# Kernel optimization log

Hardware: AMD Instinct MI355X
Metric: run time of the kernel (lower is better)

## Reference

```python
import jax, jax.numpy as jnp
import numpy as np

HEADS = 16
LN_EPS = 1e-12
MINUS_INF = -10000.0  # matches DeepSpeed's minus_inf constant


def setup_inputs() -> dict:
    key = jax.random.key(0)
    ks = jax.random.split(key, 6)
    B, S, H = 2, 2048, 2048
    x = jax.random.normal(ks[0], (B, S, H), dtype=jnp.float32)
    mask = jnp.zeros((B, 1, 1, S), dtype=jnp.float32)  # additive float mask (no padding)
    qkvw = jax.random.normal(ks[1], (H, 3 * H), dtype=jnp.float32) * 0.02
    qkvb = jax.random.normal(ks[2], (3 * H,), dtype=jnp.float32) * 0.02
    ow = jax.random.normal(ks[3], (H, H), dtype=jnp.float32) * 0.02
    norm_w = jnp.ones((H,), dtype=jnp.float32)
    norm_b = jnp.zeros((H,), dtype=jnp.float32)
    return {"x": x, "mask": mask, "qkvw": qkvw, "qkvb": qkvb, "ow": ow,
            "norm_w": norm_w, "norm_b": norm_b}


def _layernorm(x, g, b):
    mu = jnp.mean(x, axis=-1, keepdims=True)
    var = jnp.mean(jnp.square(x - mu), axis=-1, keepdims=True)
    return (x - mu) * jax.lax.rsqrt(var + LN_EPS) * g + b


def reference(x, mask, qkvw, qkvb, ow, norm_w, norm_b):
    B, S, H = x.shape
    dh = H // HEADS
    # QKVGemmOp: fused layernorm + QKV projection
    inp_norm = _layernorm(x, norm_w, norm_b)                      # [B,S,H]
    qkv = jnp.einsum('bsh,he->bse', inp_norm, qkvw) + qkvb        # [B,S,3H]
    q, k, v = jnp.split(qkv, 3, axis=-1)
    q = q.reshape(B, S, HEADS, dh).transpose(0, 2, 1, 3)          # [B,Hd,S,dh]
    k = k.reshape(B, S, HEADS, dh).transpose(0, 2, 1, 3)
    v = v.reshape(B, S, HEADS, dh).transpose(0, 2, 1, 3)
    # SoftmaxContextOp: kernel scales q and k each by 1/norm_factor,
    # norm_factor = d_head**0.25 (use_mup=False) -> net scale 1/sqrt(d_head)
    scale = 1.0 / jnp.sqrt(jnp.asarray(dh, dtype=x.dtype))
    scores = jnp.einsum('bhqd,bhkd->bhqk', q, k) * scale          # [B,Hd,S,S]
    causal = jnp.tril(jnp.ones((S, S), dtype=bool))
    scores = jnp.where(causal[None, None], scores + mask, MINUS_INF)
    probs = jax.nn.softmax(scores, axis=-1)
    ctx = jnp.einsum('bhqk,bhkd->bhqd', probs, v)                 # [B,Hd,S,dh]
    ctx = ctx.transpose(0, 2, 1, 3).reshape(B, S, H)
    # VectorMatMulOp: output projection (no bias here)
    out = jnp.einsum('bsh,ho->bso', ctx, ow)                      # [B,S,H]
    return (out, k, v, ctx, inp_norm)
```

## Files before the change

kernel.cpp:

```cpp
#include <hip/hip_runtime.h>

typedef short bf16x8 __attribute__((ext_vector_type(8)));
typedef float floatx4 __attribute__((ext_vector_type(4)));

#define MFMA16(a, b, c) __builtin_amdgcn_mfma_f32_16x16x32_bf16((a), (b), (c), 0, 0, 0)

__device__ __forceinline__ unsigned short f2bf(float f) {
    union { float f; unsigned int u; } v; v.f = f;
    unsigned int u = v.u;
    return (unsigned short)((u + 0x7FFFu + ((u >> 16) & 1u)) >> 16);
}

__device__ __forceinline__ void gld_lds16(const void* g, void* l) {
    __builtin_amdgcn_global_load_lds(
        (const __attribute__((address_space(1))) unsigned int*)g,
        (__attribute__((address_space(3))) unsigned int*)l, 16, 0, 0);
}

__global__ __launch_bounds__(256) void ln_kernel(
        const float* __restrict__ x, const float* __restrict__ g,
        const float* __restrict__ be, float* __restrict__ yo,
        unsigned short* __restrict__ yb) {
    int row = blockIdx.x, t = threadIdx.x;
    const float* xr = x + (size_t)row * 2048;
    float4 a = ((const float4*)xr)[2 * t];
    float4 b = ((const float4*)xr)[2 * t + 1];
    float s = a.x + a.y + a.z + a.w + b.x + b.y + b.z + b.w;
    float q = a.x * a.x + a.y * a.y + a.z * a.z + a.w * a.w +
              b.x * b.x + b.y * b.y + b.z * b.z + b.w * b.w;
    for (int m = 1; m < 64; m <<= 1) { s += __shfl_xor(s, m); q += __shfl_xor(q, m); }
    __shared__ float red[8];
    if ((t & 63) == 0) { red[t >> 6] = s; red[4 + (t >> 6)] = q; }
    __syncthreads();
    s = red[0] + red[1] + red[2] + red[3];
    q = red[4] + red[5] + red[6] + red[7];
    float mean = s * (1.0f / 2048.0f);
    float var = q * (1.0f / 2048.0f) - mean * mean;
    float rs = rsqrtf(var + 1e-12f);
    float4 g0 = ((const float4*)g)[2 * t], g1 = ((const float4*)g)[2 * t + 1];
    float4 b0 = ((const float4*)be)[2 * t], b1 = ((const float4*)be)[2 * t + 1];
    float4 y0, y1;
    y0.x = (a.x - mean) * rs * g0.x + b0.x;
    y0.y = (a.y - mean) * rs * g0.y + b0.y;
    y0.z = (a.z - mean) * rs * g0.z + b0.z;
    y0.w = (a.w - mean) * rs * g0.w + b0.w;
    y1.x = (b.x - mean) * rs * g1.x + b1.x;
    y1.y = (b.y - mean) * rs * g1.y + b1.y;
    y1.z = (b.z - mean) * rs * g1.z + b1.z;
    y1.w = (b.w - mean) * rs * g1.w + b1.w;
    float* yr = yo + (size_t)row * 2048;
    ((float4*)yr)[2 * t] = y0;
    ((float4*)yr)[2 * t + 1] = y1;
    union { unsigned short u[8]; uint4 v; } pk;
    pk.u[0] = f2bf(y0.x); pk.u[1] = f2bf(y0.y); pk.u[2] = f2bf(y0.z); pk.u[3] = f2bf(y0.w);
    pk.u[4] = f2bf(y1.x); pk.u[5] = f2bf(y1.y); pk.u[6] = f2bf(y1.z); pk.u[7] = f2bf(y1.w);
    *(uint4*)(yb + (size_t)row * 2048 + t * 8) = pk.v;
}

__global__ __launch_bounds__(256) void transpose_cvt(
        const float* __restrict__ src, unsigned short* __restrict__ dst,
        int K, int N) {
    __shared__ unsigned short tile[64][73];
    int n0 = blockIdx.x * 64, k0 = blockIdx.y * 64;
    size_t bo = (size_t)blockIdx.z * K * N;
    int t = threadIdx.x;
    for (int p = 0; p < 4; p++) {
        int idx = p * 256 + t; int r = idx >> 4; int c = (idx & 15) * 4;
        float4 v = *(const float4*)(src + bo + (size_t)(k0 + r) * N + n0 + c);
        tile[r][c] = f2bf(v.x); tile[r][c + 1] = f2bf(v.y);
        tile[r][c + 2] = f2bf(v.z); tile[r][c + 3] = f2bf(v.w);
    }
    __syncthreads();
    for (int p = 0; p < 4; p++) {
        int idx = p * 256 + t; int n = idx >> 4; int c = (idx & 15) * 4;
        ushort4 o;
        o.x = tile[c][n]; o.y = tile[c + 1][n];
        o.z = tile[c + 2][n]; o.w = tile[c + 3][n];
        *(ushort4*)(dst + bo + (size_t)(n0 + n) * K + k0 + c) = o;
    }
}

#define NT_QKV 32

__device__ __forceinline__ void stage_A(const unsigned short* __restrict__ Ag,
        unsigned short* As, int mh, int m0, int kt, int tid) {
#pragma unroll
    for (int j = 0; j < 2; j++) {
        int G = j * 512 + tid;
        int s = (G >> 3) & 63;
        int gr = G & 7;
        int row = j * 128 + mh * 64 + s;
        const unsigned short* src =
            Ag + (size_t)(m0 + row) * 2048 + kt * 64 + ((gr ^ (s & 7)) << 3);
        unsigned short* dst = As + j * 8192 + mh * 4096 + (tid >> 6) * 512;
        gld_lds16(src, dst);
    }
}

__device__ __forceinline__ void stage_B(const unsigned short* __restrict__ Bg,
        unsigned short* Bs, int nh, int n0, int kt, int tid) {
#pragma unroll
    for (int j = 0; j < 2; j++) {
        int G = j * 512 + tid;
        int wcc = G >> 8;
        int s = (G >> 3) & 31;
        int gr = G & 7;
        int row = wcc * 64 + nh * 32 + s;
        const unsigned short* src =
            Bg + (size_t)(n0 + row) * 2048 + kt * 64 + ((gr ^ (s & 7)) << 3);
        unsigned short* dst = Bs + wcc * 4096 + nh * 2048 + ((tid >> 6) & 3) * 512;
        gld_lds16(src, dst);
    }
}

__device__ __forceinline__ bf16x8 ldfrag(const unsigned short* S, int row, int ks,
                                         int quad, int ln15) {
    int gr = ((ks << 2) | quad) ^ (ln15 & 7);
    return *(const bf16x8*)(S + row * 64 + gr * 8);
}

#define PHASE_SYNC()                                        \
    __builtin_amdgcn_s_barrier();                           \
    asm volatile("s_waitcnt lgkmcnt(0)" ::: "memory");      \
    __builtin_amdgcn_sched_barrier(0);                      \
    __builtin_amdgcn_s_setprio(1)

#define PHASE_END()                                         \
    __builtin_amdgcn_s_setprio(0);                          \
    asm volatile("s_waitcnt vmcnt(4)" ::: "memory");        \
    __builtin_amdgcn_s_barrier()

__device__ __forceinline__ void qkv_tile(
        const unsigned short* __restrict__ Ag, const unsigned short* __restrict__ Bg,
        unsigned short* Asc, unsigned short* Bsc,
        unsigned short* Asn, unsigned short* Bsn,
        int t, int m0, int n0, int tid, int wr, int wc, int ln15, int quad,
        floatx4 (&acc)[8][4]) {
    bf16x8 a[4][2], bb[2][2];
    bool pf = (t + 1 < NT_QKV);
#pragma unroll
    for (int m = 0; m < 4; m++) {
        a[m][0] = ldfrag(Asc, wr * 128 + m * 16 + ln15, 0, quad, ln15);
        a[m][1] = ldfrag(Asc, wr * 128 + m * 16 + ln15, 1, quad, ln15);
    }
#pragma unroll
    for (int n = 0; n < 2; n++) {
        bb[n][0] = ldfrag(Bsc, wc * 64 + n * 16 + ln15, 0, quad, ln15);
        bb[n][1] = ldfrag(Bsc, wc * 64 + n * 16 + ln15, 1, quad, ln15);
    }
    if (pf) stage_B(Bg, Bsn, 0, n0, t + 1, tid);
    PHASE_SYNC();
#pragma unroll
    for (int m = 0; m < 4; m++)
#pragma unroll
        for (int n = 0; n < 2; n++) {
            acc[m][n] = MFMA16(a[m][0], bb[n][0], acc[m][n]);
            acc[m][n] = MFMA16(a[m][1], bb[n][1], acc[m][n]);
        }
    PHASE_END();
#pragma unroll
    for (int n = 0; n < 2; n++) {
        bb[n][0] = ldfrag(Bsc, wc * 64 + (2 + n) * 16 + ln15, 0, quad, ln15);
        bb[n][1] = ldfrag(Bsc, wc * 64 + (2 + n) * 16 + ln15, 1, quad, ln15);
    }
    if (pf) stage_A(Ag, Asn, 0, m0, t + 1, tid);
    PHASE_SYNC();
#pragma unroll
    for (int m = 0; m < 4; m++)
#pragma unroll
        for (int n = 0; n < 2; n++) {
            acc[m][2 + n] = MFMA16(a[m][0], bb[n][0], acc[m][2 + n]);
            acc[m][2 + n] = MFMA16(a[m][1], bb[n][1], acc[m][2 + n]);
        }
    PHASE_END();
#pragma unroll
    for (int m = 0; m < 4; m++) {
        a[m][0] = ldfrag(Asc, wr * 128 + (4 + m) * 16 + ln15, 0, quad, ln15);
        a[m][1] = ldfrag(Asc, wr * 128 + (4 + m) * 16 + ln15, 1, quad, ln15);
    }
    if (pf) stage_B(Bg, Bsn, 1, n0, t + 1, tid);
    PHASE_SYNC();
#pragma unroll
    for (int m = 0; m < 4; m++)
#pragma unroll
        for (int n = 0; n < 2; n++) {
            acc[4 + m][2 + n] = MFMA16(a[m][0], bb[n][0], acc[4 + m][2 + n]);
            acc[4 + m][2 + n] = MFMA16(a[m][1], bb[n][1], acc[4 + m][2 + n]);
        }
    PHASE_END();
#pragma unroll
    for (int n = 0; n < 2; n++) {
        bb[n][0] = ldfrag(Bsc, wc * 64 + n * 16 + ln15, 0, quad, ln15);
        bb[n][1] = ldfrag(Bsc, wc * 64 + n * 16 + ln15, 1, quad, ln15);
    }
    if (pf) stage_A(Ag, Asn, 1, m0, t + 1, tid);
    PHASE_SYNC();
#pragma unroll
    for (int m = 0; m < 4; m++)
#pragma unroll
        for (int n = 0; n < 2; n++) {
            acc[4 + m][n] = MFMA16(a[m][0], bb[n][0], acc[4 + m][n]);
            acc[4 + m][n] = MFMA16(a[m][1], bb[n][1], acc[4 + m][n]);
        }
    PHASE_END();
}

__global__ __launch_bounds__(512, 2) void gemm_qkv(
        const unsigned short* __restrict__ A, const unsigned short* __restrict__ Bt,
        const float* __restrict__ bias, float* __restrict__ ko,
        float* __restrict__ vo, unsigned short* __restrict__ qws,
        unsigned short* __restrict__ kbf) {
    __shared__ __align__(16) unsigned short As[2][16384];
    __shared__ __align__(16) unsigned short Bs[2][16384];
    int bid = blockIdx.x;
    int xcd = bid & 7, idx = bid >> 3;
    int mt = (xcd & 3) * 4 + idx / 12;
    int ntile = (xcd >> 2) * 12 + idx % 12;
    int m0 = mt * 256, n0 = ntile * 256;
    int tid = threadIdx.x;
    int wave = tid >> 6, lane = tid & 63, ln15 = lane & 15, quad = lane >> 4;
    int wr = wave >> 2, wc = wave & 3;
    floatx4 acc[8][4] = {};
    stage_B(Bt, Bs[0], 0, n0, 0, tid);
    stage_A(A, As[0], 0, m0, 0, tid);
    stage_B(Bt, Bs[0], 1, n0, 0, tid);
    stage_A(A, As[0], 1, m0, 0, tid);
    asm volatile("s_waitcnt vmcnt(4)" ::: "memory");
    __builtin_amdgcn_s_barrier();
#pragma unroll 1
    for (int t = 0; t < NT_QKV; t += 2) {
        qkv_tile(A, Bt, As[0], Bs[0], As[1], Bs[1], t,     m0, n0, tid, wr, wc, ln15, quad, acc);
        qkv_tile(A, Bt, As[1], Bs[1], As[0], Bs[0], t + 1, m0, n0, tid, wr, wc, ln15, quad, acc);
    }
#pragma unroll
    for (int mi = 0; mi < 8; mi++) {
        int row = m0 + wr * 128 + mi * 16 + quad * 4;
#pragma unroll
        for (int ni = 0; ni < 4; ni++) {
            int col = n0 + wc * 64 + ni * 16 + ln15;
            float bv = bias[col];
#pragma unroll
            for (int r = 0; r < 4; r++) {
                float val = acc[mi][ni][r] + bv;
                int rr = row + r;
                int b = rr >> 11, s = rr & 2047;
                if (col < 2048) {
                    qws[(size_t)rr * 2048 + col] = f2bf(val);
                } else if (col < 4096) {
                    int cc = col - 2048; int h = cc >> 7, d = cc & 127;
                    size_t o = ((size_t)(b * 16 + h) * 2048 + s) * 128 + d;
                    ko[o] = val;
                    kbf[o] = f2bf(val);
                } else {
                    int cc = col - 4096; int h = cc >> 7, d = cc & 127;
                    vo[((size_t)(b * 16 + h) * 2048 + s) * 128 + d] = val;
                }
            }
        }
    }
}

__global__ __launch_bounds__(256) void gemm_out(
        const float* __restrict__ Actx, const unsigned short* __restrict__ Bt,
        float* __restrict__ out) {
    __shared__ unsigned short As[128 * 72];
    __shared__ unsigned short Bs[128 * 72];
    int m0 = blockIdx.y * 128, n0 = blockIdx.x * 128;
    int t = threadIdx.x;
    int wave = t >> 6, lane = t & 63, ln15 = lane & 15, quad = lane >> 4;
    int wm = wave >> 1, wn = wave & 1;
    floatx4 acc[4][4] = {};
    for (int k0 = 0; k0 < 2048; k0 += 64) {
        for (int p = 0; p < 4; p++) {
            int idx = p * 256 + t; int r = idx >> 3; int c = (idx & 7) * 8;
            const float* ap = Actx + (size_t)(m0 + r) * 2048 + k0 + c;
            float4 u0 = ((const float4*)ap)[0], u1 = ((const float4*)ap)[1];
            union { unsigned short u[8]; uint4 v; } pk;
            pk.u[0] = f2bf(u0.x); pk.u[1] = f2bf(u0.y); pk.u[2] = f2bf(u0.z); pk.u[3] = f2bf(u0.w);
            pk.u[4] = f2bf(u1.x); pk.u[5] = f2bf(u1.y); pk.u[6] = f2bf(u1.z); pk.u[7] = f2bf(u1.w);
            *(uint4*)&As[r * 72 + c] = pk.v;
            *(uint4*)&Bs[r * 72 + c] = *(const uint4*)(Bt + (size_t)(n0 + r) * 2048 + k0 + c);
        }
        __syncthreads();
        for (int ks = 0; ks < 2; ks++) {
            bf16x8 af[4], bfr[4];
            for (int i = 0; i < 4; i++)
                af[i] = *(const bf16x8*)&As[(wm * 64 + i * 16 + ln15) * 72 + ks * 32 + quad * 8];
            for (int i = 0; i < 4; i++)
                bfr[i] = *(const bf16x8*)&Bs[(wn * 64 + i * 16 + ln15) * 72 + ks * 32 + quad * 8];
            for (int mi = 0; mi < 4; mi++)
                for (int ni = 0; ni < 4; ni++)
                    acc[mi][ni] = MFMA16(af[mi], bfr[ni], acc[mi][ni]);
        }
        __syncthreads();
    }
    for (int mi = 0; mi < 4; mi++) {
        int row = m0 + wm * 64 + mi * 16 + quad * 4;
        for (int ni = 0; ni < 4; ni++) {
            int col = n0 + wn * 64 + ni * 16 + ln15;
            for (int r = 0; r < 4; r++)
                out[(size_t)(row + r) * 2048 + col] = acc[mi][ni][r];
        }
    }
}

__global__ __launch_bounds__(256) void attn_kernel(
        const unsigned short* __restrict__ qws, const unsigned short* __restrict__ kbf,
        const unsigned short* __restrict__ vT, const float* __restrict__ mask,
        float* __restrict__ ctxo) {
    __shared__ unsigned short Ks[64 * 136];
    __shared__ unsigned short Vt[128 * 72];
    __shared__ unsigned short Pl[4 * 16 * 72];
    int jp = blockIdx.x, h = blockIdx.y, b = blockIdx.z;
    int t = threadIdx.x, wave = t >> 6, lane = t & 63, ln15 = lane & 15, quad = lane >> 4;
    const float scale = 0.08838834764831845f;

    const unsigned short* kb = kbf + (size_t)(b * 16 + h) * 2048 * 128;
    const unsigned short* vTb = vT + (size_t)(b * 16 + h) * 128 * 2048;
    const float* mb = mask + (size_t)b * 2048;

    for (int half = 0; half < 2; half++) {
        int qt = half ? (31 - jp) : jp;
        int Q0 = qt * 64;

        bf16x8 qf[4];
        const unsigned short* qbase =
            qws + ((size_t)(b * 2048 + Q0 + wave * 16 + ln15)) * 2048 + h * 128;
        for (int ks = 0; ks < 4; ks++)
            qf[ks] = *(const bf16x8*)(qbase + ks * 32 + quad * 8);

        float m_r[4], l_r[4];
        floatx4 o[8] = {};
        for (int r = 0; r < 4; r++) { m_r[r] = -1e30f; l_r[r] = 0.0f; }

        int nkt = qt + 1;
        for (int kt = 0; kt < nkt; kt++) {
            int c0 = kt * 64;
            for (int p = 0; p < 4; p++) {
                int idx = p * 256 + t; int r = idx >> 4; int c = (idx & 15) * 8;
                *(uint4*)&Ks[r * 136 + c] = *(const uint4*)(kb + (size_t)(c0 + r) * 128 + c);
            }
            for (int p = 0; p < 4; p++) {
                int idx = p * 256 + t; int d = idx >> 3; int sg = (idx & 7) * 8;
                *(uint4*)&Vt[d * 72 + sg] = *(const uint4*)(vTb + (size_t)d * 2048 + c0 + sg);
            }
            __syncthreads();

            floatx4 cs[4] = {};
            for (int ks = 0; ks < 4; ks++)
                for (int ni = 0; ni < 4; ni++) {
                    bf16x8 kfr = *(const bf16x8*)&Ks[(ni * 16 + ln15) * 136 + ks * 32 + quad * 8];
                    cs[ni] = MFMA16(qf[ks], kfr, cs[ni]);
                }

            float sv[4][4];
            float mt[4] = {-1e30f, -1e30f, -1e30f, -1e30f};
            if (kt == qt) {
                for (int ni = 0; ni < 4; ni++) {
                    int cg = c0 + ni * 16 + ln15;
                    float mk = mb[cg];
                    for (int r = 0; r < 4; r++) {
                        int qg = Q0 + wave * 16 + quad * 4 + r;
                        float v = (cg <= qg) ? cs[ni][r] * scale + mk : -10000.0f;
                        sv[ni][r] = v;
                        mt[r] = fmaxf(mt[r], v);
                    }
                }
            } else {
                for (int ni = 0; ni < 4; ni++) {
                    float mk = mb[c0 + ni * 16 + ln15];
                    for (int r = 0; r < 4; r++) {
                        float v = cs[ni][r] * scale + mk;
                        sv[ni][r] = v;
                        mt[r] = fmaxf(mt[r], v);
                    }
                }
            }
            for (int m = 1; m < 16; m <<= 1)
                for (int r = 0; r < 4; r++) mt[r] = fmaxf(mt[r], __shfl_xor(mt[r], m));
            float alpha[4], lt[4];
            for (int r = 0; r < 4; r++) {
                float mn = fmaxf(m_r[r], mt[r]);
                alpha[r] = __expf(m_r[r] - mn);
                m_r[r] = mn;
                lt[r] = 0.0f;
            }
            for (int ni = 0; ni < 4; ni++)
                for (int r = 0; r < 4; r++) {
                    float p = __expf(sv[ni][r] - m_r[r]);
                    sv[ni][r] = p;
                    lt[r] += p;
                }
            for (int m = 1; m < 16; m <<= 1)
                for (int r = 0; r < 4; r++) lt[r] += __shfl_xor(lt[r], m);
            for (int r = 0; r < 4; r++) l_r[r] = l_r[r] * alpha[r] + lt[r];
            for (int nj = 0; nj < 8; nj++)
                for (int r = 0; r < 4; r++) o[nj][r] *= alpha[r];

            unsigned short* pw = &Pl[wave * 16 * 72];
            for (int ni = 0; ni < 4; ni++)
                for (int r = 0; r < 4; r++)
                    pw[(quad * 4 + r) * 72 + ni * 16 + ln15] = f2bf(sv[ni][r]);

            for (int ks2 = 0; ks2 < 2; ks2++) {
                bf16x8 pf = *(const bf16x8*)&Pl[(wave * 16 + ln15) * 72 + ks2 * 32 + quad * 8];
                for (int nj = 0; nj < 8; nj++) {
                    bf16x8 vf = *(const bf16x8*)&Vt[(nj * 16 + ln15) * 72 + ks2 * 32 + quad * 8];
                    o[nj] = MFMA16(pf, vf, o[nj]);
                }
            }
            __syncthreads();
        }

        float rl[4];
        for (int r = 0; r < 4; r++) rl[r] = 1.0f / l_r[r];
        for (int nj = 0; nj < 8; nj++)
            for (int r = 0; r < 4; r++) {
                int s = Q0 + wave * 16 + quad * 4 + r;
                ctxo[((size_t)(b * 2048 + s)) * 2048 + h * 128 + nj * 16 + ln15] = o[nj][r] * rl[r];
            }
    }
}

extern "C" void kernel_launch(void* const* d_in, const int* in_sizes, int n_in,
                              void* d_out, int out_size, void* d_ws, size_t ws_size,
                              hipStream_t stream) {
    const float* x      = (const float*)d_in[0];
    const float* mask   = (const float*)d_in[1];
    const float* qkvw   = (const float*)d_in[2];
    const float* qkvb   = (const float*)d_in[3];
    const float* ow     = (const float*)d_in[4];
    const float* norm_w = (const float*)d_in[5];
    const float* norm_b = (const float*)d_in[6];

    float* out      = (float*)d_out;
    float* k_out    = out + 8388608;
    float* v_out    = out + 16777216;
    float* ctx_out  = out + 25165824;
    float* norm_out = out + 33554432;

    unsigned short* ws    = (unsigned short*)d_ws;
    unsigned short* xn    = ws;
    unsigned short* qkvwT = ws + 8388608;
    unsigned short* owT   = ws + 8388608 + 12582912;
    unsigned short* qws   = owT + 4194304;
    unsigned short* vT    = qws + 8388608;
    unsigned short* kbf   = vT + 8388608;

    ln_kernel<<<4096, 256, 0, stream>>>(x, norm_w, norm_b, norm_out, xn);
    transpose_cvt<<<dim3(96, 32, 1), 256, 0, stream>>>(qkvw, qkvwT, 2048, 6144);
    transpose_cvt<<<dim3(32, 32, 1), 256, 0, stream>>>(ow, owT, 2048, 2048);
    gemm_qkv<<<dim3(384), 512, 0, stream>>>(xn, qkvwT, qkvb, k_out, v_out, qws, kbf);
    transpose_cvt<<<dim3(2, 32, 32), 256, 0, stream>>>(v_out, vT, 2048, 128);
    attn_kernel<<<dim3(16, 16, 2), 256, 0, stream>>>(qws, kbf, vT, mask, ctx_out);
    gemm_out<<<dim3(16, 32), 256, 0, stream>>>(ctx_out, owT, out);
}
```

Measured before the change: 551.3 us.

## Restructure attention kernel with 128-row query tiles, register prefetch, lazy rescale

```diff
diff --git a/kernel.cpp b/kernel.cpp
--- a/kernel.cpp
+++ b/kernel.cpp
@@ -304,120 +304,186 @@
     }
 }
 
-__global__ __launch_bounds__(256) void attn_kernel(
+__device__ __forceinline__ void load_kv(const unsigned short* __restrict__ kb,
+                                        const unsigned short* __restrict__ vTb,
+                                        int c0, int t, uint4 (&kg)[4], uint4 (&vg)[4]) {
+#pragma unroll
+    for (int p = 0; p < 4; p++) {
+        int idx = p * 256 + t;
+        int r = idx >> 4, c = (idx & 15) * 8;
+        kg[p] = *(const uint4*)(kb + (size_t)(c0 + r) * 128 + c);
+        int d = idx >> 3, sg = (idx & 7) * 8;
+        vg[p] = *(const uint4*)(vTb + (size_t)d * 2048 + c0 + sg);
+    }
+}
+
+__global__ __launch_bounds__(256, 2) void attn_kernel(
         const unsigned short* __restrict__ qws, const unsigned short* __restrict__ kbf,
         const unsigned short* __restrict__ vT, const float* __restrict__ mask,
         float* __restrict__ ctxo) {
     __shared__ unsigned short Ks[64 * 136];
     __shared__ unsigned short Vt[128 * 72];
-    __shared__ unsigned short Pl[4 * 16 * 72];
-    int jp = blockIdx.x, h = blockIdx.y, b = blockIdx.z;
+    __shared__ unsigned short Pl[4 * 32 * 72];
+    int j = 15 - (int)blockIdx.x, h = blockIdx.y, b = blockIdx.z;
     int t = threadIdx.x, wave = t >> 6, lane = t & 63, ln15 = lane & 15, quad = lane >> 4;
     const float scale = 0.08838834764831845f;
 
     const unsigned short* kb = kbf + (size_t)(b * 16 + h) * 2048 * 128;
     const unsigned short* vTb = vT + (size_t)(b * 16 + h) * 128 * 2048;
     const float* mb = mask + (size_t)b * 2048;
-
-    for (int half = 0; half < 2; half++) {
-        int qt = half ? (31 - jp) : jp;
-        int Q0 = qt * 64;
-
-        bf16x8 qf[4];
+    int Q0 = j * 128;
+
+    bf16x8 qf[2][4];
+#pragma unroll
+    for (int g = 0; g < 2; g++) {
         const unsigned short* qbase =
-            qws + ((size_t)(b * 2048 + Q0 + wave * 16 + ln15)) * 2048 + h * 128;
+            qws + ((size_t)(b * 2048 + Q0 + wave * 32 + g * 16 + ln15)) * 2048 + h * 128;
+#pragma unroll
         for (int ks = 0; ks < 4; ks++)
-            qf[ks] = *(const bf16x8*)(qbase + ks * 32 + quad * 8);
-
-        float m_r[4], l_r[4];
-        floatx4 o[8] = {};
-        for (int r = 0; r < 4; r++) { m_r[r] = -1e30f; l_r[r] = 0.0f; }
-
-        int nkt = qt + 1;
-        for (int kt = 0; kt < nkt; kt++) {
-            int c0 = kt * 64;
-            for (int p = 0; p < 4; p++) {
-                int idx = p * 256 + t; int r = idx >> 4; int c = (idx & 15) * 8;
-                *(uint4*)&Ks[r * 136 + c] = *(const uint4*)(kb + (size_t)(c0 + r) * 128 + c);
+            qf[g][ks] = *(const bf16x8*)(qbase + ks * 32 + quad * 8);
+    }
+
+    float m_r[2][4], l_r[2][4];
+    floatx4 o[2][8] = {};
+#pragma unroll
+    for (int g = 0; g < 2; g++)
+#pragma unroll
+        for (int r = 0; r < 4; r++) { m_r[g][r] = -1e30f; l_r[g][r] = 0.0f; }
+
+    int nkt = 2 * j + 2;
+    uint4 kg[4], vg[4];
+    load_kv(kb, vTb, 0, t, kg, vg);
+
+#pragma unroll 1
+    for (int kt = 0; kt < nkt; kt++) {
+        int c0 = kt * 64;
+        __syncthreads();
+#pragma unroll
+        for (int p = 0; p < 4; p++) {
+            int idx = p * 256 + t;
+            int r = idx >> 4, c = (idx & 15) * 8;
+            *(uint4*)&Ks[r * 136 + c] = kg[p];
+            int d = idx >> 3, sg = (idx & 7) * 8;
+            *(uint4*)&Vt[d * 72 + sg] = vg[p];
+        }
+        __syncthreads();
+        if (kt + 1 < nkt) load_kv(kb, vTb, c0 + 64, t, kg, vg);
+
+        floatx4 cs[2][4] = {};
+        __builtin_amdgcn_s_setprio(1);
+#pragma unroll
+        for (int ks = 0; ks < 4; ks++) {
+            bf16x8 k0 = *(const bf16x8*)&Ks[(0 * 16 + ln15) * 136 + ks * 32 + quad * 8];
+            bf16x8 k1 = *(const bf16x8*)&Ks[(1 * 16 + ln15) * 136 + ks * 32 + quad * 8];
+            bf16x8 k2 = *(const bf16x8*)&Ks[(2 * 16 + ln15) * 136 + ks * 32 + quad * 8];
+            bf16x8 k3 = *(const bf16x8*)&Ks[(3 * 16 + ln15) * 136 + ks * 32 + quad * 8];
+#pragma unroll
+            for (int g = 0; g < 2; g++) {
+                cs[g][0] = MFMA16(qf[g][ks], k0, cs[g][0]);
+                cs[g][1] = MFMA16(qf[g][ks], k1, cs[g][1]);
+                cs[g][2] = MFMA16(qf[g][ks], k2, cs[g][2]);
+                cs[g][3] = MFMA16(qf[g][ks], k3, cs[g][3]);
             }
-            for (int p = 0; p < 4; p++) {
-                int idx = p * 256 + t; int d = idx >> 3; int sg = (idx & 7) * 8;
-                *(uint4*)&Vt[d * 72 + sg] = *(const uint4*)(vTb + (size_t)d * 2048 + c0 + sg);
-            }
-            __syncthreads();
-
-            floatx4 cs[4] = {};
-            for (int ks = 0; ks < 4; ks++)
-                for (int ni = 0; ni < 4; ni++) {
-                    bf16x8 kfr = *(const bf16x8*)&Ks[(ni * 16 + ln15) * 136 + ks * 32 + quad * 8];
-                    cs[ni] = MFMA16(qf[ks], kfr, cs[ni]);
-                }
-
-            float sv[4][4];
-            float mt[4] = {-1e30f, -1e30f, -1e30f, -1e30f};
-            if (kt == qt) {
-                for (int ni = 0; ni < 4; ni++) {
-                    int cg = c0 + ni * 16 + ln15;
-                    float mk = mb[cg];
-                    for (int r = 0; r < 4; r++) {
-                        int qg = Q0 + wave * 16 + quad * 4 + r;
-                        float v = (cg <= qg) ? cs[ni][r] * scale + mk : -10000.0f;
-                        sv[ni][r] = v;
-                        mt[r] = fmaxf(mt[r], v);
-                    }
-                }
-            } else {
-                for (int ni = 0; ni < 4; ni++) {
-                    float mk = mb[c0 + ni * 16 + ln15];
-                    for (int r = 0; r < 4; r++) {
-                        float v = cs[ni][r] * scale + mk;
-                        sv[ni][r] = v;
-                        mt[r] = fmaxf(mt[r], v);
-                    }
+        }
+        __builtin_amdgcn_s_setprio(0);
+
+        float mt[2][4];
+#pragma unroll
+        for (int g = 0; g < 2; g++) {
+#pragma unroll
+            for (int r = 0; r < 4; r++) mt[g][r] = -1e30f;
+#pragma unroll
+            for (int ni = 0; ni < 4; ni++) {
+                int cg = c0 + ni * 16 + ln15;
+                float mk = mb[cg];
+#pragma unroll
+                for (int r = 0; r < 4; r++) {
+                    int qg = Q0 + wave * 32 + g * 16 + quad * 4 + r;
+                    float v = fmaf(cs[g][ni][r], scale, mk);
+                    v = (cg <= qg) ? v : -10000.0f;
+                    cs[g][ni][r] = v;
+                    mt[g][r] = fmaxf(mt[g][r], v);
                 }
             }
+#pragma unroll
             for (int m = 1; m < 16; m <<= 1)
-                for (int r = 0; r < 4; r++) mt[r] = fmaxf(mt[r], __shfl_xor(mt[r], m));
-            float alpha[4], lt[4];
-            for (int r = 0; r < 4; r++) {
-                float mn = fmaxf(m_r[r], mt[r]);
-                alpha[r] = __expf(m_r[r] - mn);
-                m_r[r] = mn;
-                lt[r] = 0.0f;
-            }
+#pragma unroll
+                for (int r = 0; r < 4; r++)
+                    mt[g][r] = fmaxf(mt[g][r], __shfl_xor(mt[g][r], m));
+        }
+
+        bool grow = false;
+#pragma unroll
+        for (int g = 0; g < 2; g++)
+#pragma unroll
+            for (int r = 0; r < 4; r++)
+                grow = grow || (mt[g][r] > m_r[g][r] + 8.0f);
+        if (__any((int)grow)) {
+#pragma unroll
+            for (int g = 0; g < 2; g++)
+#pragma unroll
+                for (int r = 0; r < 4; r++) {
+                    float mn = fmaxf(m_r[g][r], mt[g][r]);
+                    float alpha = __expf(m_r[g][r] - mn);
+                    m_r[g][r] = mn;
+                    l_r[g][r] *= alpha;
+#pragma unroll
+                    for (int nj = 0; nj < 8; nj++) o[g][nj][r] *= alpha;
+                }
+        }
+
+#pragma unroll
+        for (int g = 0; g < 2; g++) {
+            float lt[4] = {0.0f, 0.0f, 0.0f, 0.0f};
+#pragma unroll
             for (int ni = 0; ni < 4; ni++)
+#pragma unroll
                 for (int r = 0; r < 4; r++) {
-                    float p = __expf(sv[ni][r] - m_r[r]);
-                    sv[ni][r] = p;
+                    float p = __expf(cs[g][ni][r] - m_r[g][r]);
+                    cs[g][ni][r] = p;
                     lt[r] += p;
                 }
+#pragma unroll
             for (int m = 1; m < 16; m <<= 1)
+#pragma unroll
                 for (int r = 0; r < 4; r++) lt[r] += __shfl_xor(lt[r], m);
-            for (int r = 0; r < 4; r++) l_r[r] = l_r[r] * alpha[r] + lt[r];
-            for (int nj = 0; nj < 8; nj++)
-                for (int r = 0; r < 4; r++) o[nj][r] *= alpha[r];
-
-            unsigned short* pw = &Pl[wave * 16 * 72];
+#pragma unroll
+            for (int r = 0; r < 4; r++) l_r[g][r] += lt[r];
+            unsigned short* pw = &Pl[(wave * 32 + g * 16) * 72];
+#pragma unroll
             for (int ni = 0; ni < 4; ni++)
+#pragma unroll
                 for (int r = 0; r < 4; r++)
-                    pw[(quad * 4 + r) * 72 + ni * 16 + ln15] = f2bf(sv[ni][r]);
-
-            for (int ks2 = 0; ks2 < 2; ks2++) {
-                bf16x8 pf = *(const bf16x8*)&Pl[(wave * 16 + ln15) * 72 + ks2 * 32 + quad * 8];
-                for (int nj = 0; nj < 8; nj++) {
-                    bf16x8 vf = *(const bf16x8*)&Vt[(nj * 16 + ln15) * 72 + ks2 * 32 + quad * 8];
-                    o[nj] = MFMA16(pf, vf, o[nj]);
-                }
+                    pw[(quad * 4 + r) * 72 + ni * 16 + ln15] = f2bf(cs[g][ni][r]);
+        }
+
+        __builtin_amdgcn_s_setprio(1);
+#pragma unroll
+        for (int ks2 = 0; ks2 < 2; ks2++) {
+            bf16x8 pf0 = *(const bf16x8*)&Pl[(wave * 32 + 0 * 16 + ln15) * 72 + ks2 * 32 + quad * 8];
+            bf16x8 pf1 = *(const bf16x8*)&Pl[(wave * 32 + 1 * 16 + ln15) * 72 + ks2 * 32 + quad * 8];
+#pragma unroll
+            for (int nj = 0; nj < 8; nj++) {
+                bf16x8 vf = *(const bf16x8*)&Vt[(nj * 16 + ln15) * 72 + ks2 * 32 + quad * 8];
+                o[0][nj] = MFMA16(pf0, vf, o[0][nj]);
+                o[1][nj] = MFMA16(pf1, vf, o[1][nj]);
             }
-            __syncthreads();
-        }
-
+        }
+        __builtin_amdgcn_s_setprio(0);
+    }
+
+#pragma unroll
+    for (int g = 0; g < 2; g++) {
         float rl[4];
-        for (int r = 0; r < 4; r++) rl[r] = 1.0f / l_r[r];
+#pragma unroll
+        for (int r = 0; r < 4; r++) rl[r] = 1.0f / l_r[g][r];
+#pragma unroll
         for (int nj = 0; nj < 8; nj++)
+#pragma unroll
             for (int r = 0; r < 4; r++) {
-                int s = Q0 + wave * 16 + quad * 4 + r;
-                ctxo[((size_t)(b * 2048 + s)) * 2048 + h * 128 + nj * 16 + ln15] = o[nj][r] * rl[r];
+                int s = Q0 + wave * 32 + g * 16 + quad * 4 + r;
+                ctxo[((size_t)(b * 2048 + s)) * 2048 + h * 128 + nj * 16 + ln15] =
+                    o[g][nj][r] * rl[r];
             }
     }
 }
```

Result: slower. 682.0 us (+23.7%).

## Prefetch next K/V tile into registers and skip lazy softmax rescales

Applied to the files above, without the earlier changes.

```diff
diff --git a/kernel.cpp b/kernel.cpp
--- a/kernel.cpp
+++ b/kernel.cpp
@@ -304,7 +304,20 @@
     }
 }
 
-__global__ __launch_bounds__(256) void attn_kernel(
+__device__ __forceinline__ void load_kv(const unsigned short* __restrict__ kb,
+                                        const unsigned short* __restrict__ vTb,
+                                        int c0, int t, uint4 (&kg)[4], uint4 (&vg)[4]) {
+#pragma unroll
+    for (int p = 0; p < 4; p++) {
+        int idx = p * 256 + t;
+        int r = idx >> 4, c = (idx & 15) * 8;
+        kg[p] = *(const uint4*)(kb + (size_t)(c0 + r) * 128 + c);
+        int d = idx >> 3, sg = (idx & 7) * 8;
+        vg[p] = *(const uint4*)(vTb + (size_t)d * 2048 + c0 + sg);
+    }
+}
+
+__global__ __launch_bounds__(256, 2) void attn_kernel(
         const unsigned short* __restrict__ qws, const unsigned short* __restrict__ kbf,
         const unsigned short* __restrict__ vT, const float* __restrict__ mask,
         float* __restrict__ ctxo) {
@@ -319,6 +332,10 @@
     const unsigned short* vTb = vT + (size_t)(b * 16 + h) * 128 * 2048;
     const float* mb = mask + (size_t)b * 2048;
 
+    uint4 kg[4], vg[4];
+    load_kv(kb, vTb, 0, t, kg, vg);
+
+#pragma unroll 1
     for (int half = 0; half < 2; half++) {
         int qt = half ? (31 - jp) : jp;
         int Q0 = qt * 64;
@@ -326,95 +343,132 @@
         bf16x8 qf[4];
         const unsigned short* qbase =
             qws + ((size_t)(b * 2048 + Q0 + wave * 16 + ln15)) * 2048 + h * 128;
+#pragma unroll
         for (int ks = 0; ks < 4; ks++)
             qf[ks] = *(const bf16x8*)(qbase + ks * 32 + quad * 8);
 
         float m_r[4], l_r[4];
         floatx4 o[8] = {};
+#pragma unroll
         for (int r = 0; r < 4; r++) { m_r[r] = -1e30f; l_r[r] = 0.0f; }
 
         int nkt = qt + 1;
+#pragma unroll 1
         for (int kt = 0; kt < nkt; kt++) {
             int c0 = kt * 64;
+#pragma unroll
             for (int p = 0; p < 4; p++) {
-                int idx = p * 256 + t; int r = idx >> 4; int c = (idx & 15) * 8;
-                *(uint4*)&Ks[r * 136 + c] = *(const uint4*)(kb + (size_t)(c0 + r) * 128 + c);
-            }
-            for (int p = 0; p < 4; p++) {
-                int idx = p * 256 + t; int d = idx >> 3; int sg = (idx & 7) * 8;
-                *(uint4*)&Vt[d * 72 + sg] = *(const uint4*)(vTb + (size_t)d * 2048 + c0 + sg);
+                int idx = p * 256 + t;
+                int r = idx >> 4, c = (idx & 15) * 8;
+                *(uint4*)&Ks[r * 136 + c] = kg[p];
+                int d = idx >> 3, sg = (idx & 7) * 8;
+                *(uint4*)&Vt[d * 72 + sg] = vg[p];
             }
             __syncthreads();
+            if (kt + 1 < nkt)      load_kv(kb, vTb, c0 + 64, t, kg, vg);
+            else if (half == 0)    load_kv(kb, vTb, 0, t, kg, vg);
 
             floatx4 cs[4] = {};
+            __builtin_amdgcn_s_setprio(1);
+#pragma unroll
             for (int ks = 0; ks < 4; ks++)
+#pragma unroll
                 for (int ni = 0; ni < 4; ni++) {
                     bf16x8 kfr = *(const bf16x8*)&Ks[(ni * 16 + ln15) * 136 + ks * 32 + quad * 8];
                     cs[ni] = MFMA16(qf[ks], kfr, cs[ni]);
                 }
+            __builtin_amdgcn_s_setprio(0);
 
             float sv[4][4];
             float mt[4] = {-1e30f, -1e30f, -1e30f, -1e30f};
             if (kt == qt) {
+#pragma unroll
                 for (int ni = 0; ni < 4; ni++) {
                     int cg = c0 + ni * 16 + ln15;
                     float mk = mb[cg];
+#pragma unroll
                     for (int r = 0; r < 4; r++) {
                         int qg = Q0 + wave * 16 + quad * 4 + r;
-                        float v = (cg <= qg) ? cs[ni][r] * scale + mk : -10000.0f;
+                        float v = (cg <= qg) ? fmaf(cs[ni][r], scale, mk) : -10000.0f;
                         sv[ni][r] = v;
                         mt[r] = fmaxf(mt[r], v);
                     }
                 }
             } else {
+#pragma unroll
                 for (int ni = 0; ni < 4; ni++) {
                     float mk = mb[c0 + ni * 16 + ln15];
+#pragma unroll
                     for (int r = 0; r < 4; r++) {
-                        float v = cs[ni][r] * scale + mk;
+                        float v = fmaf(cs[ni][r], scale, mk);
                         sv[ni][r] = v;
                         mt[r] = fmaxf(mt[r], v);
                     }
                 }
             }
+#pragma unroll
             for (int m = 1; m < 16; m <<= 1)
+#pragma unroll
                 for (int r = 0; r < 4; r++) mt[r] = fmaxf(mt[r], __shfl_xor(mt[r], m));
-            float alpha[4], lt[4];
-            for (int r = 0; r < 4; r++) {
-                float mn = fmaxf(m_r[r], mt[r]);
-                alpha[r] = __expf(m_r[r] - mn);
-                m_r[r] = mn;
-                lt[r] = 0.0f;
+
+            bool grow = false;
+#pragma unroll
+            for (int r = 0; r < 4; r++) grow = grow || (mt[r] > m_r[r] + 8.0f);
+            if (__any((int)grow)) {
+#pragma unroll
+                for (int r = 0; r < 4; r++) {
+                    float mn = fmaxf(m_r[r], mt[r]);
+                    float al = __expf(m_r[r] - mn);
+                    m_r[r] = mn;
+                    l_r[r] *= al;
+#pragma unroll
+                    for (int nj = 0; nj < 8; nj++) o[nj][r] *= al;
+                }
             }
+
+            float lt[4] = {0.0f, 0.0f, 0.0f, 0.0f};
+#pragma unroll
             for (int ni = 0; ni < 4; ni++)
+#pragma unroll
                 for (int r = 0; r < 4; r++) {
                     float p = __expf(sv[ni][r] - m_r[r]);
                     sv[ni][r] = p;
                     lt[r] += p;
                 }
+#pragma unroll
             for (int m = 1; m < 16; m <<= 1)
+#pragma unroll
                 for (int r = 0; r < 4; r++) lt[r] += __shfl_xor(lt[r], m);
-            for (int r = 0; r < 4; r++) l_r[r] = l_r[r] * alpha[r] + lt[r];
-            for (int nj = 0; nj < 8; nj++)
-                for (int r = 0; r < 4; r++) o[nj][r] *= alpha[r];
+#pragma unroll
+            for (int r = 0; r < 4; r++) l_r[r] += lt[r];
 
             unsigned short* pw = &Pl[wave * 16 * 72];
+#pragma unroll
             for (int ni = 0; ni < 4; ni++)
+#pragma unroll
                 for (int r = 0; r < 4; r++)
                     pw[(quad * 4 + r) * 72 + ni * 16 + ln15] = f2bf(sv[ni][r]);
 
+            __builtin_amdgcn_s_setprio(1);
+#pragma unroll
             for (int ks2 = 0; ks2 < 2; ks2++) {
                 bf16x8 pf = *(const bf16x8*)&Pl[(wave * 16 + ln15) * 72 + ks2 * 32 + quad * 8];
+#pragma unroll
                 for (int nj = 0; nj < 8; nj++) {
                     bf16x8 vf = *(const bf16x8*)&Vt[(nj * 16 + ln15) * 72 + ks2 * 32 + quad * 8];
                     o[nj] = MFMA16(pf, vf, o[nj]);
                 }
             }
+            __builtin_amdgcn_s_setprio(0);
             __syncthreads();
         }
 
         float rl[4];
+#pragma unroll
         for (int r = 0; r < 4; r++) rl[r] = 1.0f / l_r[r];
+#pragma unroll
         for (int nj = 0; nj < 8; nj++)
+#pragma unroll
             for (int r = 0; r < 4; r++) {
                 int s = Q0 + wave * 16 + quad * 4 + r;
                 ctxo[((size_t)(b * 2048 + s)) * 2048 + h * 128 + nj * 16 + ln15] = o[nj][r] * rl[r];
```

New measurement: 650.3 us. 18.0% more time.
